# Kernel optimization log

Hardware: AMD Instinct MI355X
Metric: run time of the kernel (lower is better)

Reference implementation:

```python
import jax, jax.numpy as jnp
import numpy as np

NUM_HEAD = 16


def setup_inputs() -> dict:
    key = jax.random.key(0)
    ks = jax.random.split(key, 4)
    B, C, D = 2, 2048, 1024
    hidden_states = jax.random.normal(ks[0], (B, C, D), dtype=jnp.float32)
    attention_mask = jnp.zeros((B, 1, C, C), dtype=jnp.float32)
    Wqkv = jax.random.normal(ks[1], (D, 3 * D), dtype=jnp.float32) * (D ** -0.5)
    bqkv = jnp.zeros((3 * D,), dtype=jnp.float32)
    Wo = jax.random.normal(ks[2], (D, D), dtype=jnp.float32) * (D ** -0.5)
    bo = jnp.zeros((D,), dtype=jnp.float32)
    return {"hidden_states": hidden_states, "attention_mask": attention_mask,
            "Wqkv": Wqkv, "bqkv": bqkv, "Wo": Wo, "bo": bo}


def reference(hidden_states, attention_mask, Wqkv, bqkv, Wo, bo):
    B, C, D = hidden_states.shape
    H = NUM_HEAD
    hd = D // H
    scaling = hd ** -0.5

    qkv = hidden_states @ Wqkv + bqkv                      # [B, C, 3D]
    q, k, v = jnp.split(qkv, 3, axis=-1)
    # [B, C, H, hd] -> [B, H, C, hd]
    q = q.reshape(B, C, H, hd).transpose(0, 2, 1, 3)
    k = k.reshape(B, C, H, hd).transpose(0, 2, 1, 3)
    v = v.reshape(B, C, H, hd).transpose(0, 2, 1, 3)

    scores = jnp.einsum("bhqd,bhkd->bhqk", q, k) * scaling  # [B, H, C, C]
    causal = jnp.tril(jnp.ones((C, C), dtype=bool))[None, None]
    mask = jnp.where(causal, attention_mask, -jnp.inf)      # [B, 1, C, C]
    probs = jax.nn.softmax(scores + mask, axis=-1)
    out = jnp.einsum("bhqk,bhkd->bhqd", probs, v)           # [B, H, C, hd]
    out = out.transpose(0, 2, 1, 3).reshape(B, C, D)
    return out @ Wo + bo
```

## Files before the change

kernel.cpp:

```cpp
#include <hip/hip_runtime.h>
#include <hip/hip_bf16.h>
#include <cstdint>
#include <cstddef>

typedef __attribute__((ext_vector_type(8))) short short8;
typedef __attribute__((ext_vector_type(4))) float f32x4;
typedef __attribute__((ext_vector_type(16))) float f32x16;
typedef unsigned short u16;
typedef unsigned int u32;

#define B_ 2
#define C_ 2048
#define D_ 1024
#define H_ 16
#define HD_ 64

static __device__ __forceinline__ u16 f2b(float f) {
  u32 x = __builtin_bit_cast(u32, f);
  x += 0x7FFFu + ((x >> 16) & 1u);
  return (u16)(x >> 16);
}
static __device__ __forceinline__ float b2f(u16 v) {
  return __builtin_bit_cast(float, (u32)v << 16);
}

__global__ void k_convert(const float* __restrict__ in, u16* __restrict__ out, int n) {
  int i = (blockIdx.x * blockDim.x + threadIdx.x) * 4;
  const int stride = gridDim.x * blockDim.x * 4;
  for (; i < n; i += stride) {
    float4 v = *reinterpret_cast<const float4*>(in + i);
    ushort4 o;
    o.x = f2b(v.x); o.y = f2b(v.y); o.z = f2b(v.z); o.w = f2b(v.w);
    *reinterpret_cast<ushort4*>(out + i) = o;
  }
}

__global__ void k_tconv(const float* __restrict__ in, u16* __restrict__ out, int R, int Cc) {
  __shared__ float tile[64][65];
  const int tC = blockIdx.x * 64;
  const int tR = blockIdx.y * 64;
  const int t = threadIdx.x;
  const int r0 = t >> 4;
  const int c0 = (t & 15) * 4;
#pragma unroll
  for (int ii = 0; ii < 4; ++ii) {
    int r = ii * 16 + r0;
    float4 v = *reinterpret_cast<const float4*>(&in[(size_t)(tR + r) * Cc + tC + c0]);
    tile[r][c0] = v.x; tile[r][c0 + 1] = v.y; tile[r][c0 + 2] = v.z; tile[r][c0 + 3] = v.w;
  }
  __syncthreads();
#pragma unroll
  for (int ii = 0; ii < 4; ++ii) {
    int c = ii * 16 + r0;
    ushort4 o;
    o.x = f2b(tile[c0 + 0][c]);
    o.y = f2b(tile[c0 + 1][c]);
    o.z = f2b(tile[c0 + 2][c]);
    o.w = f2b(tile[c0 + 3][c]);
    *reinterpret_cast<ushort4*>(&out[(size_t)(tC + c) * R + tR + c0]) = o;
  }
}

__global__ void k_maskflags(const float* __restrict__ mask, u32* __restrict__ flags) {
  const int bid = blockIdx.x;
  const int kt = bid & 31, qs = (bid >> 5) & 31, b = bid >> 10;
  const int t = threadIdx.x;
  const float* base = mask + ((size_t)b * C_ + qs * 64) * C_ + kt * 64;
  const int row = t >> 2, c0 = (t & 3) * 16;
  int any = 0;
#pragma unroll
  for (int i = 0; i < 4; ++i) {
    float4 v = *reinterpret_cast<const float4*>(base + (size_t)row * C_ + c0 + i * 4);
    any |= (v.x != 0.f) | (v.y != 0.f) | (v.z != 0.f) | (v.w != 0.f);
  }
  __shared__ int sh[4];
  const unsigned long long bal = __ballot(any);
  if ((t & 63) == 0) sh[t >> 6] = (bal != 0ull);
  __syncthreads();
  if (t == 0) flags[bid] = (u32)(sh[0] | sh[1] | sh[2] | sh[3]);
}

#define GLL16(gptr, lptr) __builtin_amdgcn_global_load_lds( \
    (const __attribute__((address_space(1))) u32*)(gptr),   \
    (__attribute__((address_space(3))) u32*)(lptr), 16, 0, 0)

template<int EPI, int BM>
__global__ __launch_bounds__(256) void k_gemm(
    const u16* __restrict__ A, const u16* __restrict__ Bt,
    int M, int N, int K, const float* __restrict__ bias,
    u16* __restrict__ Cq, u16* __restrict__ Ck, u16* __restrict__ Cv,
    float* __restrict__ Cf)
{
  constexpr int WCW = (BM == 128) ? 64 : 32;
  constexpr int NF = WCW / 16;
  __shared__ __align__(16) u16 As[BM * 64];
  __shared__ __align__(16) u16 Bs[128 * 64];
  const int t = threadIdx.x;
  const int l = t & 63, w = t >> 6;
  const int wr = (BM == 128) ? (w >> 1) : 0;
  const int wc = (BM == 128) ? (w & 1) : w;
  const int lr = l & 15, lg = l >> 4;
  const int swk = lr & 7;
  const int m0 = blockIdx.y * BM, n0 = blockIdx.x * 128;
  f32x4 acc[4][NF] = {};

  for (int k0 = 0; k0 < K; k0 += 64) {
#pragma unroll
    for (int s = 0; s < BM / 32; ++s) {
      const int u = s * 256 + t;
      const int row = u >> 3, slot = (u & 7) ^ (row & 7);
      GLL16(A + (size_t)(m0 + row) * K + k0 + (slot << 3), As + (u << 3));
    }
#pragma unroll
    for (int s = 0; s < 4; ++s) {
      const int u = s * 256 + t;
      const int row = u >> 3, slot = (u & 7) ^ (row & 7);
      GLL16(Bt + (size_t)(n0 + row) * K + k0 + (slot << 3), Bs + (u << 3));
    }
    __syncthreads();
    short8 af[2][4], bfr[2][NF];
#pragma unroll
    for (int s = 0; s < 2; ++s) {
#pragma unroll
      for (int m = 0; m < 4; ++m)
        af[s][m] = *reinterpret_cast<const short8*>(
            &As[((wr * 64 + m * 16 + lr) << 6) + (((s * 4 + lg) ^ swk) << 3)]);
#pragma unroll
      for (int n = 0; n < NF; ++n)
        bfr[s][n] = *reinterpret_cast<const short8*>(
            &Bs[((wc * WCW + n * 16 + lr) << 6) + (((s * 4 + lg) ^ swk) << 3)]);
    }
#pragma unroll
    for (int s = 0; s < 2; ++s)
#pragma unroll
      for (int m = 0; m < 4; ++m)
#pragma unroll
        for (int n = 0; n < NF; ++n)
          acc[m][n] = __builtin_amdgcn_mfma_f32_16x16x32_bf16(af[s][m], bfr[s][n], acc[m][n], 0, 0, 0);
    __syncthreads();
  }

#pragma unroll
  for (int m = 0; m < 4; ++m) {
    const int mg = m0 + wr * 64 + m * 16 + lg * 4;
    const int bq = mg >> 11, c0 = mg & 2047;
#pragma unroll
    for (int n = 0; n < NF; ++n) {
      const int ng = n0 + wc * WCW + n * 16 + lr;
      const float bia = bias[ng];
      if (EPI == 0) {
        const int reg = ng >> 10, d = ng & 1023, h = d >> 6, e = d & 63;
        if (reg == 2) {
          u16* vp = Cv + (((size_t)(bq * H_ + h) * HD_ + e) << 11) + c0;
#pragma unroll
          for (int j = 0; j < 4; ++j) vp[j] = f2b(acc[m][n][j] + bia);
        } else {
          u16* dst = (reg == 0) ? Cq : Ck;
#pragma unroll
          for (int j = 0; j < 4; ++j)
            dst[(((size_t)(bq * H_ + h) * C_ + c0 + j) << 6) + e] = f2b(acc[m][n][j] + bia);
        }
      } else {
#pragma unroll
        for (int j = 0; j < 4; ++j)
          Cf[(size_t)(mg + j) * N + ng] = acc[m][n][j] + bia;
      }
    }
  }
}

static __device__ __forceinline__ void stage_kv(
    const u16* __restrict__ Kbh, const u16* __restrict__ Vbh,
    u16* Kd, u16* Vd, int kt, int t)
{
#pragma unroll
  for (int ch = 0; ch < 2; ++ch) {
    const int u = ch * 256 + t;
    const int row = u >> 3, slot = (u & 7) ^ (row & 7);
    GLL16(Kbh + (((size_t)(kt * 64 + row)) << 6) + (slot << 3), Kd + (u << 3));
    GLL16(Vbh + (((size_t)row) << 11) + kt * 64 + (slot << 3), Vd + (u << 3));
  }
}

__global__ __launch_bounds__(256) void k_attn(
    const u16* __restrict__ Q, const u16* __restrict__ Kb, const u16* __restrict__ Vt,
    const float* __restrict__ mask, const u32* __restrict__ flags,
    u16* __restrict__ O, u16* __restrict__ Opart, float2* __restrict__ ml)
{
  __shared__ __align__(16) u16 Kl[2][64 * 64];
  __shared__ __align__(16) u16 Vl[2][64 * 64];
  __shared__ __align__(16) u16 Sc[4][2304];
  const int bid = blockIdx.x;
  const int bh = bid & 31;
  const int sidx = 23 - (bid >> 5);
  int qt, seg, nseg;
  if (sidx < 8) { qt = sidx; seg = 0; nseg = 1; }
  else          { const int u = sidx - 8; qt = 8 + (u >> 1); seg = u & 1; nseg = 2; }
  const int ntiles = 2 * qt + 2;
  const int kt0 = seg * 16;
  const int kt1 = seg ? ntiles : ((ntiles < 16) ? ntiles : 16);
  const int slot = ((bh << 3) + (qt - 8)) * 2 + seg;

  const int b = bh >> 4, h = bh & 15;
  const int t = threadIdx.x;
  const int l = t & 63, w = t >> 6;
  const int q = l & 31, hi = l >> 5;
  const int q7 = q & 7;

  const u16* Kbh = Kb + (size_t)bh * (C_ * HD_);
  const u16* Vbh = Vt + (size_t)bh * (HD_ * C_);
  char* Swb = reinterpret_cast<char*>(Sc[w]);

  const int q0w = qt * 128 + w * 32;
  const int qg = q0w + q;
  const int qmaxw = q0w + 31;

  short8 aq[4];
  {
    const u16* qp = Q + ((size_t)bh * C_ + qg) * HD_ + hi * 8;
#pragma unroll
    for (int kh = 0; kh < 4; ++kh) {
      short8 v = *reinterpret_cast<const short8*>(qp + kh * 16);
#pragma unroll
      for (int i = 0; i < 8; ++i) {
        const float f = b2f((u16)v[i]) * 0.125f;
        v[i] = (short)f2b(f);
      }
      aq[kh] = v;
    }
  }

  f32x16 oa0 = {}, oa1 = {};
  float mrun = -INFINITY, srun = 0.f;
  const float* mrow = mask + ((size_t)b * C_ + qg) * C_;
  const u32* fb = flags + (size_t)(b * 32 + (q0w >> 6)) * 32;

  stage_kv(Kbh, Vbh, Kl[0], Vl[0], kt0, t);

#pragma unroll 1
  for (int kt = kt0; kt < kt1; ++kt) {
    const int cur = kt & 1;
    __syncthreads();
    if (kt + 1 < kt1) stage_kv(Kbh, Vbh, Kl[cur ^ 1], Vl[cur ^ 1], kt + 1, t);
    if (kt * 64 > qmaxw) continue;

    const char* Kc = reinterpret_cast<const char*>(Kl[cur]);
    const char* Vc = reinterpret_cast<const char*>(Vl[cur]);

    f32x16 p0 = {}, p1 = {};
#pragma unroll
    for (int kh = 0; kh < 4; ++kh) {
      const int sl = ((2 * kh + hi) ^ q7) << 4;
      const short8 k0 = *reinterpret_cast<const short8*>(Kc + q * 128 + sl);
      const short8 k1 = *reinterpret_cast<const short8*>(Kc + (32 + q) * 128 + sl);
      p0 = __builtin_amdgcn_mfma_f32_32x32x16_bf16(k0, aq[kh], p0, 0, 0, 0);
      p1 = __builtin_amdgcn_mfma_f32_32x32x16_bf16(k1, aq[kh], p1, 0, 0, 0);
    }

    if (fb[kt]) {
      const float* mp = mrow + kt * 64 + 4 * hi;
#pragma unroll
      for (int g = 0; g < 4; ++g) {
        const float4 m0 = *reinterpret_cast<const float4*>(mp + 8 * g);
        const float4 m1 = *reinterpret_cast<const float4*>(mp + 32 + 8 * g);
        p0[4*g+0] += m0.x; p0[4*g+1] += m0.y; p0[4*g+2] += m0.z; p0[4*g+3] += m0.w;
        p1[4*g+0] += m1.x; p1[4*g+1] += m1.y; p1[4*g+2] += m1.z; p1[4*g+3] += m1.w;
      }
    }
    if (kt * 64 + 63 > q0w) {
#pragma unroll
      for (int r = 0; r < 16; ++r) {
        const int kl = kt * 64 + (r & 3) + 8 * (r >> 2) + 4 * hi;
        if (kl > qg) p0[r] = -INFINITY;
        if (kl + 32 > qg) p1[r] = -INFINITY;
      }
    }

    float pm = -INFINITY;
#pragma unroll
    for (int r = 0; r < 16; ++r) pm = fmaxf(pm, fmaxf(p0[r], p1[r]));
    pm = fmaxf(pm, __shfl_xor(pm, 32));
    const float mn = fmaxf(fmaxf(mrun, pm), -1e30f);
    const float rs = __expf(mrun - mn);
    float sum = 0.f;
#pragma unroll
    for (int r = 0; r < 16; ++r) {
      p0[r] = __expf(p0[r] - mn); sum += p0[r];
      p1[r] = __expf(p1[r] - mn); sum += p1[r];
    }
    sum += __shfl_xor(sum, 32);
    srun = srun * rs + sum;
    mrun = mn;
    oa0 *= rs; oa1 *= rs;

#pragma unroll
    for (int g = 0; g < 4; ++g) {
#pragma unroll
      for (int m = 0; m < 2; ++m) {
        u32 w0, w1;
        asm("v_cvt_pk_bf16_f32 %0, %1, %2" : "=v"(w0) : "v"(p0[4*g+2*m]), "v"(p0[4*g+2*m+1]));
        asm("v_cvt_pk_bf16_f32 %0, %1, %2" : "=v"(w1) : "v"(p1[4*g+2*m]), "v"(p1[4*g+2*m+1]));
        *reinterpret_cast<u32*>(Swb + q * 128 + ((g ^ q7) << 4) + 8 * hi + 4 * m) = w0;
        *reinterpret_cast<u32*>(Swb + q * 128 + (((4 + g) ^ q7) << 4) + 8 * hi + 4 * m) = w1;
      }
    }
    asm volatile("" ::: "memory");

#pragma unroll
    for (int ks = 0; ks < 4; ++ks) {
      const int sl = ((2 * ks + hi) ^ q7) << 4;
      const short8 bp = *reinterpret_cast<const short8*>(Swb + q * 128 + sl);
      const short8 v0 = *reinterpret_cast<const short8*>(Vc + q * 128 + sl);
      const short8 v1 = *reinterpret_cast<const short8*>(Vc + (32 + q) * 128 + sl);
      oa0 = __builtin_amdgcn_mfma_f32_32x32x16_bf16(v0, bp, oa0, 0, 0, 0);
      oa1 = __builtin_amdgcn_mfma_f32_32x32x16_bf16(v1, bp, oa1, 0, 0, 0);
    }
  }

  const float rinv = 1.f / srun;
#pragma unroll
  for (int g = 0; g < 4; ++g) {
    const int d0 = 8 * g + 4 * hi;
    const float a0 = oa0[4*g+0] * rinv, a1 = oa0[4*g+1] * rinv;
    const float a2 = oa0[4*g+2] * rinv, a3 = oa0[4*g+3] * rinv;
    const float b0 = oa1[4*g+0] * rinv, b1 = oa1[4*g+1] * rinv;
    const float b2 = oa1[4*g+2] * rinv, b3 = oa1[4*g+3] * rinv;
    u32 w0, w1, w2, w3;
    asm("v_cvt_pk_bf16_f32 %0, %1, %2" : "=v"(w0) : "v"(a0), "v"(a1));
    asm("v_cvt_pk_bf16_f32 %0, %1, %2" : "=v"(w1) : "v"(a2), "v"(a3));
    asm("v_cvt_pk_bf16_f32 %0, %1, %2" : "=v"(w2) : "v"(b0), "v"(b1));
    asm("v_cvt_pk_bf16_f32 %0, %1, %2" : "=v"(w3) : "v"(b2), "v"(b3));
    *reinterpret_cast<uint2*>(Swb + q * 144 + d0 * 2) = make_uint2(w0, w1);
    *reinterpret_cast<uint2*>(Swb + q * 144 + (d0 + 32) * 2) = make_uint2(w2, w3);
  }
  asm volatile("" ::: "memory");
  const int q2 = l >> 1, hf = l & 1;
  if (nseg == 1) {
    u16* orow = O + ((size_t)b * C_ + q0w + q2) * D_ + h * 64 + hf * 32;
#pragma unroll
    for (int i = 0; i < 4; ++i) {
      const short8 v = *reinterpret_cast<const short8*>(Swb + q2 * 144 + hf * 64 + i * 16);
      *reinterpret_cast<short8*>(orow + i * 8) = v;
    }
  } else {
    u16* prow = Opart + (((size_t)slot * 128 + w * 32 + q2) << 6) + hf * 32;
#pragma unroll
    for (int i = 0; i < 4; ++i) {
      const short8 v = *reinterpret_cast<const short8*>(Swb + q2 * 144 + hf * 64 + i * 16);
      *reinterpret_cast<short8*>(prow + i * 8) = v;
    }
    if (hi == 0) ml[(size_t)slot * 128 + w * 32 + q] = make_float2(mrun, srun);
  }
}

__global__ __launch_bounds__(256) void k_merge(
    const u16* __restrict__ Opart, const float2* __restrict__ ml, u16* __restrict__ O)
{
  const int bid = blockIdx.x;
  const int bh = bid & 31;
  const int qt = 8 + (bid >> 5);
  const int slot0 = ((bh << 3) + (qt - 8)) * 2;
  const int b = bh >> 4, h = bh & 15;
  const int t = threadIdx.x;
  const int q = t >> 1, dh = t & 1;

  const float2 v0 = ml[(size_t)slot0 * 128 + q];
  const float2 v1 = ml[(size_t)(slot0 + 1) * 128 + q];
  const float M = fmaxf(v0.x, v1.x);
  const float a0 = __expf(v0.x - M) * v0.y;
  const float a1 = __expf(v1.x - M) * v1.y;
  const float rT = 1.f / (a0 + a1);
  const float r0 = a0 * rT, r1 = a1 * rT;

  const u16* p0 = Opart + (((size_t)slot0 * 128 + q) << 6) + dh * 32;
  const u16* p1 = Opart + (((size_t)(slot0 + 1) * 128 + q) << 6) + dh * 32;
  u16* orow = O + ((size_t)b * C_ + qt * 128 + q) * D_ + h * 64 + dh * 32;
#pragma unroll
  for (int i = 0; i < 4; ++i) {
    const short8 x0 = *reinterpret_cast<const short8*>(p0 + i * 8);
    const short8 x1 = *reinterpret_cast<const short8*>(p1 + i * 8);
    short8 y;
#pragma unroll
    for (int j = 0; j < 8; ++j)
      y[j] = (short)f2b(r0 * b2f((u16)x0[j]) + r1 * b2f((u16)x1[j]));
    *reinterpret_cast<short8*>(orow + i * 8) = y;
  }
}

extern "C" void kernel_launch(void* const* d_in, const int* in_sizes, int n_in,
                              void* d_out, int out_size, void* d_ws, size_t ws_size,
                              hipStream_t stream) {
  const float* hs   = (const float*)d_in[0];
  const float* mask = (const float*)d_in[1];
  const float* Wqkv = (const float*)d_in[2];
  const float* bqkv = (const float*)d_in[3];
  const float* Wo   = (const float*)d_in[4];
  const float* bo   = (const float*)d_in[5];
  float* out = (float*)d_out;
  char* ws = (char*)d_ws;

  u16*    hsb   = (u16*)(ws);
  u16*    Opart = (u16*)(ws);
  u16*    Wqkvt = (u16*)(ws + (8  << 20));
  float2* mlbuf = (float2*)(ws + (19 << 20));
  u32*    flags = (u32*)(ws + (20 << 20) + (1 << 19));
  u16*    Wot   = (u16*)(ws + (21 << 20));
  u16*    Qb    = (u16*)(ws + (24 << 20));
  u16*    Kb    = (u16*)(ws + (32 << 20));
  u16*    Vtb   = (u16*)(ws + (40 << 20));
  u16*    AOb   = (u16*)(ws + (48 << 20));

  k_convert<<<2048, 256, 0, stream>>>(hs, hsb, 4096 * 1024);
  k_tconv<<<dim3(3072 / 64, 1024 / 64), 256, 0, stream>>>(Wqkv, Wqkvt, 1024, 3072);
  k_tconv<<<dim3(1024 / 64, 1024 / 64), 256, 0, stream>>>(Wo, Wot, 1024, 1024);
  k_maskflags<<<2048, 256, 0, stream>>>(mask, flags);
  k_gemm<0, 128><<<dim3(24, 32), 256, 0, stream>>>(hsb, Wqkvt, 4096, 3072, 1024, bqkv,
                                                   Qb, Kb, Vtb, nullptr);
  k_attn<<<768, 256, 0, stream>>>(Qb, Kb, Vtb, mask, flags, AOb, Opart, mlbuf);
  k_merge<<<256, 256, 0, stream>>>(Opart, mlbuf, AOb);
  k_gemm<1, 64><<<dim3(8, 64), 256, 0, stream>>>(AOb, Wot, 4096, 1024, 1024, bo,
                                                 nullptr, nullptr, nullptr, out);
}
```

Before: 127.8 us.

## Rebalance causal attention split into 12-tile segments and keep P in registers

Replaces the 2-way KV split with a table-driven schedule that cuts longer query tiles into up to three 12-tile segments, so work is spread more evenly across 960 blocks, and extends the merge kernel to combine up to three partials. Softmax moves to the base-2 domain by folding log2(e) into the Q scaling and the mask add, and rescaling is skipped when no lane's running max grows. The probability tile is passed to the PV MFMA through v_permlane32_swap in registers instead of a round trip through LDS, and s_setprio raises priority around the MFMA block. The risks are more partial writes and merge traffic, plus some precision change from folding log2(e) into bf16 Q.

```diff
diff --git a/kernel.cpp b/kernel.cpp
--- a/kernel.cpp
+++ b/kernel.cpp
@@ -6,6 +6,7 @@
 typedef __attribute__((ext_vector_type(8))) short short8;
 typedef __attribute__((ext_vector_type(4))) float f32x4;
 typedef __attribute__((ext_vector_type(16))) float f32x16;
+typedef __attribute__((ext_vector_type(4))) unsigned int u32x4;
 typedef unsigned short u16;
 typedef unsigned int u32;
 
@@ -14,6 +15,7 @@
 #define D_ 1024
 #define H_ 16
 #define HD_ 64
+#define LOG2E 1.4426950408889634f
 
 static __device__ __forceinline__ u16 f2b(float f) {
   u32 x = __builtin_bit_cast(u32, f);
@@ -23,6 +25,10 @@
 static __device__ __forceinline__ float b2f(u16 v) {
   return __builtin_bit_cast(float, (u32)v << 16);
 }
+
+__device__ const unsigned char SEGTAB[30] = {
+  207, 223, 206, 222, 205, 221, 204, 220, 139, 155, 138, 137, 136, 135, 134, 69,
+  154, 68, 239, 153, 67, 238, 152, 66, 237, 151, 65, 236, 150, 64};
 
 __global__ void k_convert(const float* __restrict__ in, u16* __restrict__ out, int n) {
   int i = (blockIdx.x * blockDim.x + threadIdx.x) * 4;
@@ -192,14 +198,12 @@
   __shared__ __align__(16) u16 Sc[4][2304];
   const int bid = blockIdx.x;
   const int bh = bid & 31;
-  const int sidx = 23 - (bid >> 5);
-  int qt, seg, nseg;
-  if (sidx < 8) { qt = sidx; seg = 0; nseg = 1; }
-  else          { const int u = sidx - 8; qt = 8 + (u >> 1); seg = u & 1; nseg = 2; }
+  const int e = SEGTAB[bid >> 5];
+  const int qt = e & 15, seg = (e >> 4) & 3, nseg = e >> 6;
   const int ntiles = 2 * qt + 2;
-  const int kt0 = seg * 16;
-  const int kt1 = seg ? ntiles : ((ntiles < 16) ? ntiles : 16);
-  const int slot = ((bh << 3) + (qt - 8)) * 2 + seg;
+  const int kt0 = seg * 12;
+  const int kt1 = (kt0 + 12 < ntiles) ? kt0 + 12 : ntiles;
+  const int slot = (bh * 10 + (qt - 6)) * 3 + seg;
 
   const int b = bh >> 4, h = bh & 15;
   const int t = threadIdx.x;
@@ -223,7 +227,7 @@
       short8 v = *reinterpret_cast<const short8*>(qp + kh * 16);
 #pragma unroll
       for (int i = 0; i < 8; ++i) {
-        const float f = b2f((u16)v[i]) * 0.125f;
+        const float f = b2f((u16)v[i]) * (0.125f * LOG2E);
         v[i] = (short)f2b(f);
       }
       aq[kh] = v;
@@ -263,8 +267,14 @@
       for (int g = 0; g < 4; ++g) {
         const float4 m0 = *reinterpret_cast<const float4*>(mp + 8 * g);
         const float4 m1 = *reinterpret_cast<const float4*>(mp + 32 + 8 * g);
-        p0[4*g+0] += m0.x; p0[4*g+1] += m0.y; p0[4*g+2] += m0.z; p0[4*g+3] += m0.w;
-        p1[4*g+0] += m1.x; p1[4*g+1] += m1.y; p1[4*g+2] += m1.z; p1[4*g+3] += m1.w;
+        p0[4*g+0] = fmaf(m0.x, LOG2E, p0[4*g+0]);
+        p0[4*g+1] = fmaf(m0.y, LOG2E, p0[4*g+1]);
+        p0[4*g+2] = fmaf(m0.z, LOG2E, p0[4*g+2]);
+        p0[4*g+3] = fmaf(m0.w, LOG2E, p0[4*g+3]);
+        p1[4*g+0] = fmaf(m1.x, LOG2E, p1[4*g+0]);
+        p1[4*g+1] = fmaf(m1.y, LOG2E, p1[4*g+1]);
+        p1[4*g+2] = fmaf(m1.z, LOG2E, p1[4*g+2]);
+        p1[4*g+3] = fmaf(m1.w, LOG2E, p1[4*g+3]);
       }
     }
     if (kt * 64 + 63 > q0w) {
@@ -280,41 +290,49 @@
 #pragma unroll
     for (int r = 0; r < 16; ++r) pm = fmaxf(pm, fmaxf(p0[r], p1[r]));
     pm = fmaxf(pm, __shfl_xor(pm, 32));
-    const float mn = fmaxf(fmaxf(mrun, pm), -1e30f);
-    const float rs = __expf(mrun - mn);
+    if (__ballot(pm > mrun) != 0ull) {
+      const float mn = fmaxf(fmaxf(mrun, pm), -1e30f);
+      const float rs = exp2f(mrun - mn);
+      srun *= rs;
+      oa0 *= rs; oa1 *= rs;
+      mrun = mn;
+    }
     float sum = 0.f;
 #pragma unroll
     for (int r = 0; r < 16; ++r) {
-      p0[r] = __expf(p0[r] - mn); sum += p0[r];
-      p1[r] = __expf(p1[r] - mn); sum += p1[r];
+      p0[r] = exp2f(p0[r] - mrun); sum += p0[r];
+      p1[r] = exp2f(p1[r] - mrun); sum += p1[r];
     }
     sum += __shfl_xor(sum, 32);
-    srun = srun * rs + sum;
-    mrun = mn;
-    oa0 *= rs; oa1 *= rs;
-
-#pragma unroll
-    for (int g = 0; g < 4; ++g) {
-#pragma unroll
-      for (int m = 0; m < 2; ++m) {
-        u32 w0, w1;
-        asm("v_cvt_pk_bf16_f32 %0, %1, %2" : "=v"(w0) : "v"(p0[4*g+2*m]), "v"(p0[4*g+2*m+1]));
-        asm("v_cvt_pk_bf16_f32 %0, %1, %2" : "=v"(w1) : "v"(p1[4*g+2*m]), "v"(p1[4*g+2*m+1]));
-        *reinterpret_cast<u32*>(Swb + q * 128 + ((g ^ q7) << 4) + 8 * hi + 4 * m) = w0;
-        *reinterpret_cast<u32*>(Swb + q * 128 + (((4 + g) ^ q7) << 4) + 8 * hi + 4 * m) = w1;
+    srun += sum;
+
+    __builtin_amdgcn_s_setprio(1);
+#pragma unroll
+    for (int ks = 0; ks < 4; ++ks) {
+      const int o = (ks & 1) * 8;
+      u32 X, X2, Y, Y2;
+      if (ks < 2) {
+        asm("v_cvt_pk_bf16_f32 %0, %1, %2" : "=v"(X)  : "v"(p0[o+0]), "v"(p0[o+1]));
+        asm("v_cvt_pk_bf16_f32 %0, %1, %2" : "=v"(X2) : "v"(p0[o+2]), "v"(p0[o+3]));
+        asm("v_cvt_pk_bf16_f32 %0, %1, %2" : "=v"(Y)  : "v"(p0[o+4]), "v"(p0[o+5]));
+        asm("v_cvt_pk_bf16_f32 %0, %1, %2" : "=v"(Y2) : "v"(p0[o+6]), "v"(p0[o+7]));
+      } else {
+        asm("v_cvt_pk_bf16_f32 %0, %1, %2" : "=v"(X)  : "v"(p1[o+0]), "v"(p1[o+1]));
+        asm("v_cvt_pk_bf16_f32 %0, %1, %2" : "=v"(X2) : "v"(p1[o+2]), "v"(p1[o+3]));
+        asm("v_cvt_pk_bf16_f32 %0, %1, %2" : "=v"(Y)  : "v"(p1[o+4]), "v"(p1[o+5]));
+        asm("v_cvt_pk_bf16_f32 %0, %1, %2" : "=v"(Y2) : "v"(p1[o+6]), "v"(p1[o+7]));
       }
-    }
-    asm volatile("" ::: "memory");
-
-#pragma unroll
-    for (int ks = 0; ks < 4; ++ks) {
+      asm("v_permlane32_swap_b32 %0, %1" : "+v"(X), "+v"(Y));
+      asm("v_permlane32_swap_b32 %0, %1" : "+v"(X2), "+v"(Y2));
+      const u32x4 bw = {X, X2, Y, Y2};
+      const short8 bp = __builtin_bit_cast(short8, bw);
       const int sl = ((2 * ks + hi) ^ q7) << 4;
-      const short8 bp = *reinterpret_cast<const short8*>(Swb + q * 128 + sl);
       const short8 v0 = *reinterpret_cast<const short8*>(Vc + q * 128 + sl);
       const short8 v1 = *reinterpret_cast<const short8*>(Vc + (32 + q) * 128 + sl);
       oa0 = __builtin_amdgcn_mfma_f32_32x32x16_bf16(v0, bp, oa0, 0, 0, 0);
       oa1 = __builtin_amdgcn_mfma_f32_32x32x16_bf16(v1, bp, oa1, 0, 0, 0);
     }
+    __builtin_amdgcn_s_setprio(0);
   }
 
   const float rinv = 1.f / srun;
@@ -358,32 +376,45 @@
 {
   const int bid = blockIdx.x;
   const int bh = bid & 31;
-  const int qt = 8 + (bid >> 5);
-  const int slot0 = ((bh << 3) + (qt - 8)) * 2;
+  const int qt = 6 + (bid >> 5);
+  const int nseg = (qt >= 12) ? 3 : 2;
+  const int slot0 = (bh * 10 + (qt - 6)) * 3;
   const int b = bh >> 4, h = bh & 15;
   const int t = threadIdx.x;
   const int q = t >> 1, dh = t & 1;
 
-  const float2 v0 = ml[(size_t)slot0 * 128 + q];
-  const float2 v1 = ml[(size_t)(slot0 + 1) * 128 + q];
-  const float M = fmaxf(v0.x, v1.x);
-  const float a0 = __expf(v0.x - M) * v0.y;
-  const float a1 = __expf(v1.x - M) * v1.y;
-  const float rT = 1.f / (a0 + a1);
-  const float r0 = a0 * rT, r1 = a1 * rT;
-
-  const u16* p0 = Opart + (((size_t)slot0 * 128 + q) << 6) + dh * 32;
-  const u16* p1 = Opart + (((size_t)(slot0 + 1) * 128 + q) << 6) + dh * 32;
+  float m[3], l_[3];
+  float M = -INFINITY;
+#pragma unroll 3
+  for (int s = 0; s < nseg; ++s) {
+    const float2 v = ml[(size_t)(slot0 + s) * 128 + q];
+    m[s] = v.x; l_[s] = v.y;
+    M = fmaxf(M, v.x);
+  }
+  float a[3], L = 0.f;
+#pragma unroll 3
+  for (int s = 0; s < nseg; ++s) { a[s] = exp2f(m[s] - M) * l_[s]; L += a[s]; }
+  const float rL = 1.f / L;
+
+  float acc[32] = {};
+#pragma unroll 3
+  for (int s = 0; s < nseg; ++s) {
+    const u16* op = Opart + (((size_t)(slot0 + s) * 128 + q) << 6) + dh * 32;
+    const float ws = a[s] * rL;
+#pragma unroll
+    for (int i = 0; i < 4; ++i) {
+      const short8 v = *reinterpret_cast<const short8*>(op + i * 8);
+#pragma unroll
+      for (int j = 0; j < 8; ++j) acc[i * 8 + j] += ws * b2f((u16)v[j]);
+    }
+  }
   u16* orow = O + ((size_t)b * C_ + qt * 128 + q) * D_ + h * 64 + dh * 32;
 #pragma unroll
   for (int i = 0; i < 4; ++i) {
-    const short8 x0 = *reinterpret_cast<const short8*>(p0 + i * 8);
-    const short8 x1 = *reinterpret_cast<const short8*>(p1 + i * 8);
-    short8 y;
-#pragma unroll
-    for (int j = 0; j < 8; ++j)
-      y[j] = (short)f2b(r0 * b2f((u16)x0[j]) + r1 * b2f((u16)x1[j]));
-    *reinterpret_cast<short8*>(orow + i * 8) = y;
+    short8 v;
+#pragma unroll
+    for (int j = 0; j < 8; ++j) v[j] = (short)f2b(acc[i * 8 + j]);
+    *reinterpret_cast<short8*>(orow + i * 8) = v;
   }
 }
 
@@ -416,8 +447,8 @@
   k_maskflags<<<2048, 256, 0, stream>>>(mask, flags);
   k_gemm<0, 128><<<dim3(24, 32), 256, 0, stream>>>(hsb, Wqkvt, 4096, 3072, 1024, bqkv,
                                                    Qb, Kb, Vtb, nullptr);
-  k_attn<<<768, 256, 0, stream>>>(Qb, Kb, Vtb, mask, flags, AOb, Opart, mlbuf);
-  k_merge<<<256, 256, 0, stream>>>(Opart, mlbuf, AOb);
+  k_attn<<<960, 256, 0, stream>>>(Qb, Kb, Vtb, mask, flags, AOb, Opart, mlbuf);
+  k_merge<<<320, 256, 0, stream>>>(Opart, mlbuf, AOb);
   k_gemm<1, 64><<<dim3(8, 64), 256, 0, stream>>>(AOb, Wot, 4096, 1024, 1024, bo,
                                                  nullptr, nullptr, nullptr, out);
 }
```

Result: slower. 132.6 us (+3.7%).
